# Kernel optimization log

Hardware: AMD Instinct MI355X
Metric: run time of the kernel (lower is better)

The kernel has to match this reference:

```python
import jax, jax.numpy as jnp
import numpy as np

D_BINS = 59          # cfg.cam_d
BEV_H, BEV_W = 128, 128


def setup_inputs() -> dict:
    key = jax.random.key(0)
    k = jax.random.split(key, 7)
    B, N, Cin, H, W = 4, 6, 256, 16, 44
    C = 80  # cfg.cam_bev_c
    img_feats = jax.random.normal(k[0], (B, N, Cin, H, W), dtype=jnp.float32)
    rots = jax.random.normal(k[1], (B, N, 3, 3), dtype=jnp.float32)
    trans = jax.random.normal(k[2], (B, N, 3), dtype=jnp.float32)
    intrins = jax.random.normal(k[3], (B, N, 3, 3), dtype=jnp.float32)
    # 1x1 conv == per-pixel linear layer: weight (D+C, Cin), bias (D+C,)
    w_depth = jax.random.normal(k[4], (D_BINS + C, Cin), dtype=jnp.float32) / np.sqrt(Cin)
    b_depth = jnp.zeros((D_BINS + C,), dtype=jnp.float32)
    # projected BEV grid indices (what get_geometry produces via randint)
    geom = jax.random.randint(k[5], (B, N, D_BINS, H, W, 2), 0, BEV_H, dtype=jnp.int32)
    return {"img_feats": img_feats, "rots": rots, "trans": trans,
            "intrins": intrins, "w_depth": w_depth, "b_depth": b_depth,
            "geom": geom}


def reference(img_feats, rots, trans, intrins, w_depth, b_depth, geom):
    B, N, Cin, H, W = img_feats.shape
    C = w_depth.shape[0] - D_BINS
    # depth_net: 1x1 conv -> (B, N, D+C, H, W)
    x = jnp.einsum('bnchw,oc->bnohw', img_feats, w_depth) + b_depth[None, None, :, None, None]
    depth = jax.nn.softmax(x[:, :, :D_BINS], axis=2)          # (B,N,D,H,W)
    context = x[:, :, D_BINS:]                                 # (B,N,C,H,W)
    # outer product: (B,N,D,C,H,W) -> (B,N,D,H,W,C)
    frustum = depth[:, :, :, None] * context[:, :, None]
    frustum = jnp.transpose(frustum, (0, 1, 2, 4, 5, 3))
    # voxel pooling: scatter-add frustum points into BEV grid by geom indices
    cell = geom[..., 0] * BEV_W + geom[..., 1]                 # (B,N,D,H,W)
    flat_idx = (jnp.arange(B, dtype=jnp.int32)[:, None] * (BEV_H * BEV_W)
                + cell.reshape(B, -1)).reshape(-1)
    bev = jax.ops.segment_sum(frustum.reshape(-1, C), flat_idx,
                              num_segments=B * BEV_H * BEV_W)
    return bev.reshape(B, BEV_H, BEV_W, C).transpose(0, 3, 1, 2)  # (B,C,bev_h,bev_w)
```

## Files before the change

kernel.cpp:

```cpp
#include <hip/hip_runtime.h>
#include <hip/hip_bf16.h>
#include <math.h>

#define D_BINS 59
#define CTX    80
#define O_TOT  139
#define K_CIN  256
#define PIXELS 704
#define BNPAIR 24
#define BEVHW  16384
#define NBATCH 4

#define NTILE   128
#define NBUCKET (NBATCH * NTILE)
#define TCELLS  128

#define NBLK    264
#define SEGS    66
#define EPB     (64 * D_BINS)

#define CAP     2816
#define CAPP    (CAP + TCELLS * 7)

#define CTX_OFF    0
#define CTX_F      (BNPAIR * PIXELS * CTX / 2)
#define CNTMAT_OFF (CTX_OFF + CTX_F)
#define OFSMAT_OFF (CNTMAT_OFF + NBLK * NTILE)
#define PLIST_OFF  (OFSMAT_OFF + NBLK * NTILE)

__global__ __launch_bounds__(256) void gemm_fused(
    const float* __restrict__ img,
    const float* __restrict__ w,
    const float* __restrict__ bias,
    const int*   __restrict__ geom,
    __hip_bfloat16* __restrict__ ctx,
    uint2*       __restrict__ plist,
    int*         __restrict__ cntmat,
    int*         __restrict__ ofsmat)
{
    __shared__ float As[16][64];
    __shared__ float Bs[16][64];
    __shared__ float red[16][64];
    __shared__ int lh[NTILE], lofs[NTILE], lcur[NTILE], sscan[NTILE];

    const int tid = threadIdx.x;
    const int tx  = tid & 15;
    const int ty  = tid >> 4;
    const int bn  = blockIdx.z;
    const int by  = blockIdx.y;
    const int o0  = by * 64;
    const int p0  = blockIdx.x * 64;

    const float* imgbn = img + (size_t)bn * K_CIN * PIXELS;

    float acc[4][4];
#pragma unroll
    for (int i = 0; i < 4; ++i)
#pragma unroll
        for (int j = 0; j < 4; ++j) acc[i][j] = 0.f;

    const int a_ol = tid >> 2;
    const int a_kc = (tid & 3) * 4;
    const int b_kl = tid >> 4;
    const int b_p4 = (tid & 15) * 4;

    for (int kt = 0; kt < K_CIN; kt += 16) {
        {
            const int o = o0 + a_ol;
            float4 v = make_float4(0.f, 0.f, 0.f, 0.f);
            if (o < O_TOT) v = *(const float4*)&w[(size_t)o * K_CIN + kt + a_kc];
            As[a_kc + 0][a_ol] = v.x;
            As[a_kc + 1][a_ol] = v.y;
            As[a_kc + 2][a_ol] = v.z;
            As[a_kc + 3][a_ol] = v.w;
        }
        *(float4*)&Bs[b_kl][b_p4] =
            *(const float4*)&imgbn[(size_t)(kt + b_kl) * PIXELS + p0 + b_p4];
        __syncthreads();

#pragma unroll
        for (int kk = 0; kk < 16; ++kk) {
            const float4 a = *(const float4*)&As[kk][ty * 4];
            const float4 b = *(const float4*)&Bs[kk][tx * 4];
            const float av[4] = {a.x, a.y, a.z, a.w};
            const float bv[4] = {b.x, b.y, b.z, b.w};
#pragma unroll
            for (int i = 0; i < 4; ++i)
#pragma unroll
                for (int j = 0; j < 4; ++j)
                    acc[i][j] += av[i] * bv[j];
        }
        __syncthreads();
    }

    if (by == 0) {
        float bvv[4];
#pragma unroll
        for (int i = 0; i < 4; ++i) bvv[i] = bias[ty * 4 + i];
#pragma unroll
        for (int i = 0; i < 4; ++i)
#pragma unroll
            for (int j = 0; j < 4; ++j) acc[i][j] += bvv[i];

        float pm[4] = {-INFINITY, -INFINITY, -INFINITY, -INFINITY};
#pragma unroll
        for (int i = 0; i < 4; ++i) {
            if (ty * 4 + i < D_BINS) {
#pragma unroll
                for (int j = 0; j < 4; ++j) pm[j] = fmaxf(pm[j], acc[i][j]);
            }
        }
#pragma unroll
        for (int j = 0; j < 4; ++j) red[ty][tx * 4 + j] = pm[j];
        __syncthreads();
        float gm[4] = {-INFINITY, -INFINITY, -INFINITY, -INFINITY};
        for (int t = 0; t < 15; ++t) {
            const float4 r = *(const float4*)&red[t][tx * 4];
            gm[0] = fmaxf(gm[0], r.x); gm[1] = fmaxf(gm[1], r.y);
            gm[2] = fmaxf(gm[2], r.z); gm[3] = fmaxf(gm[3], r.w);
        }
        __syncthreads();
        float ps[4] = {0.f, 0.f, 0.f, 0.f};
#pragma unroll
        for (int i = 0; i < 4; ++i) {
            if (ty * 4 + i < D_BINS) {
#pragma unroll
                for (int j = 0; j < 4; ++j) {
                    const float e = __expf(acc[i][j] - gm[j]);
                    acc[i][j] = e;
                    ps[j] += e;
                }
            }
        }
#pragma unroll
        for (int j = 0; j < 4; ++j) red[ty][tx * 4 + j] = (ty < 15) ? ps[j] : 0.f;
        if (tid < NTILE) lh[tid] = 0;
        __syncthreads();
        float gs[4] = {0.f, 0.f, 0.f, 0.f};
        for (int t = 0; t < 15; ++t) {
            const float4 r = *(const float4*)&red[t][tx * 4];
            gs[0] += r.x; gs[1] += r.y; gs[2] += r.z; gs[3] += r.w;
        }
        float inv[4];
#pragma unroll
        for (int j = 0; j < 4; ++j) inv[j] = 1.f / gs[j];

        const int2* g2 = (const int2*)geom;
        unsigned bc[4][4];
#pragma unroll
        for (int i = 0; i < 4; ++i) {
            const int o = ty * 4 + i;
            if (o < D_BINS) {
                const size_t gidx = ((size_t)(bn * D_BINS + o)) * PIXELS + p0 + tx * 4;
                const int4 ga = *(const int4*)&g2[gidx];
                const int4 gb = *(const int4*)&g2[gidx + 2];
                const int gx[4] = {ga.x, ga.z, gb.x, gb.z};
                const int gy[4] = {ga.y, ga.w, gb.y, gb.w};
#pragma unroll
                for (int j = 0; j < 4; ++j) {
                    const int tile = (gx[j] >> 3) * 8 + (gy[j] >> 4);
                    const int cell = (gx[j] & 7) * 16 + (gy[j] & 15);
                    bc[i][j] = (unsigned)((tile << 7) | cell);
                    atomicAdd(&lh[tile], 1);
                }
            }
        }
        __syncthreads();

        if (tid < NTILE) sscan[tid] = lh[tid];
        __syncthreads();
#pragma unroll
        for (int off = 1; off < NTILE; off <<= 1) {
            const int t = (tid < NTILE && tid >= off) ? sscan[tid - off] : 0;
            __syncthreads();
            if (tid < NTILE) sscan[tid] += t;
            __syncthreads();
        }
        const int blk = bn * 11 + blockIdx.x;
        if (tid < NTILE) {
            const int excl = sscan[tid] - lh[tid];
            lofs[tid] = excl;
            lcur[tid] = 0;
            cntmat[(size_t)blk * NTILE + tid] = lh[tid];
            ofsmat[(size_t)blk * NTILE + tid] = excl;
        }
        __syncthreads();

        uint2* dst = plist + (size_t)blk * EPB;
#pragma unroll
        for (int j = 0; j < 4; ++j) {
            const unsigned ctxoff = (unsigned)((bn * PIXELS + p0 + tx * 4 + j) * CTX);
#pragma unroll
            for (int i = 0; i < 4; ++i) {
                const int o = ty * 4 + i;
                if (o < D_BINS) {
                    const unsigned u = bc[i][j];
                    const int t = (int)(u >> 7);
                    const int pos = lofs[t] + atomicAdd(&lcur[t], 1);
                    dst[pos] = make_uint2(__float_as_uint(acc[i][j] * inv[j]),
                                          (ctxoff << 7) | (u & 127u));
                }
            }
        }

#pragma unroll
        for (int i = 0; i < 4; ++i) {
            const int o = ty * 4 + i;
            if (o >= D_BINS) {
                const int c = o - D_BINS;
                __hip_bfloat16* cdst = ctx + ((size_t)bn * PIXELS + p0 + tx * 4) * CTX + c;
#pragma unroll
                for (int j = 0; j < 4; ++j)
                    cdst[(size_t)j * CTX] = __float2bfloat16(acc[i][j]);
            }
        }
    } else {
#pragma unroll
        for (int i = 0; i < 4; ++i) {
            const int o = o0 + ty * 4 + i;
            if (o >= O_TOT) continue;
            const float bvv = bias[o];
            const int c = o - D_BINS;
            __hip_bfloat16* cdst = ctx + ((size_t)bn * PIXELS + p0 + tx * 4) * CTX + c;
#pragma unroll
            for (int j = 0; j < 4; ++j)
                cdst[(size_t)j * CTX] = __float2bfloat16(acc[i][j] + bvv);
        }
    }
}

__global__ __launch_bounds__(1024) void gather_kernel(
    const uint2* __restrict__ plist,
    const int*   __restrict__ cntmat,
    const int*   __restrict__ ofsmat,
    const unsigned short* __restrict__ ctx,
    float*       __restrict__ out)
{
    __shared__ float sacc[CTX][TCELLS + 1];
    __shared__ uint2 bufB[CAPP];
    __shared__ int sg[128];
    __shared__ int segcnt[SEGS], segofs[SEGS];
    __shared__ int cellcnt[TCELLS], celloff[TCELLS], cellcur[TCELLS], sc[TCELLS];
    uint2* bufA = (uint2*)sacc;

    const int tid    = threadIdx.x;
    const int wv     = tid >> 6;
    const int lane   = tid & 63;
    const int bucket = blockIdx.x;
    const int b      = bucket >> 7;
    const int tile   = bucket & 127;
    const int blk0   = b * SEGS;

    if (tid < 128) {
        const int c = (tid < SEGS) ? cntmat[(size_t)(blk0 + tid) * NTILE + tile] : 0;
        sg[tid] = c;
        if (tid < SEGS) segcnt[tid] = c;
    }
    __syncthreads();
#pragma unroll
    for (int off = 1; off < 128; off <<= 1) {
        const int t = (tid < 128 && tid >= off) ? sg[tid - off] : 0;
        __syncthreads();
        if (tid < 128) sg[tid] += t;
        __syncthreads();
    }
    if (tid < SEGS) segofs[tid] = sg[tid] - segcnt[tid];
    __syncthreads();
    const int total = sg[127];

    for (int sgi = wv; sgi < SEGS; sgi += 16) {
        const int n = segcnt[sgi];
        if (!n) continue;
        const int dstb = segofs[sgi];
        const uint2* sp = plist + (size_t)(blk0 + sgi) * EPB
                          + ofsmat[(size_t)(blk0 + sgi) * NTILE + tile];
        for (int i = lane; i < n; i += 64) {
            const int d = dstb + i;
            if (d < CAP) bufA[d] = sp[i];
        }
    }
    const int ncap = (total < CAP) ? total : CAP;
    __syncthreads();

    if (tid < TCELLS) cellcnt[tid] = 0;
    __syncthreads();
    for (int i = tid; i < ncap; i += 1024)
        atomicAdd(&cellcnt[bufA[i].y & 127u], 1);
    __syncthreads();
    if (tid < TCELLS) sc[tid] = (cellcnt[tid] + 7) & ~7;
    __syncthreads();
#pragma unroll
    for (int off = 1; off < TCELLS; off <<= 1) {
        const int t = (tid < TCELLS && tid >= off) ? sc[tid - off] : 0;
        __syncthreads();
        if (tid < TCELLS) sc[tid] += t;
        __syncthreads();
    }
    if (tid < TCELLS) {
        celloff[tid] = sc[tid] - ((cellcnt[tid] + 7) & ~7);
        cellcur[tid] = 0;
    }
    __syncthreads();
    const int padtotal = sc[TCELLS - 1];
    for (int i = tid; i < padtotal; i += 1024) bufB[i] = make_uint2(0u, 0u);
    __syncthreads();
    for (int i = tid; i < ncap; i += 1024) {
        const uint2 e = bufA[i];
        const int c = (int)(e.y & 127u);
        bufB[celloff[c] + atomicAdd(&cellcur[c], 1)] = e;
    }
    __syncthreads();

    for (int c = wv; c < TCELLS; c += 16) {
        const int s0 = celloff[c];
        const int pc = (cellcnt[c] + 7) & ~7;
        float a0 = 0.f, a1 = 0.f;
        for (int i = 0; i < pc; i += 8) {
            uint2 e[8];
#pragma unroll
            for (int r = 0; r < 8; ++r) e[r] = bufB[s0 + i + r];
            if (lane < 40) {
                unsigned u[8];
#pragma unroll
                for (int r = 0; r < 8; ++r)
                    u[r] = *(const unsigned*)(ctx + (e[r].y >> 7) + 2 * lane);
#pragma unroll
                for (int r = 0; r < 8; ++r) {
                    const float d  = __uint_as_float(e[r].x);
                    const float f0 = __uint_as_float(u[r] << 16);
                    const float f1 = __uint_as_float(u[r] & 0xffff0000u);
                    a0 += d * f0;
                    a1 += d * f1;
                }
            }
        }
        if (lane < 40) {
            sacc[2 * lane][c]     = a0;
            sacc[2 * lane + 1][c] = a1;
        }
    }

    if (total > CAP) {
        for (int sgi = 0; sgi < SEGS; ++sgi) {
            const int dstb = segofs[sgi];
            const int n    = segcnt[sgi];
            if (dstb + n <= CAP) continue;
            const uint2* sp = plist + (size_t)(blk0 + sgi) * EPB
                              + ofsmat[(size_t)(blk0 + sgi) * NTILE + tile];
            const int i0 = (CAP > dstb) ? (CAP - dstb) : 0;
            for (int i = i0; i < n; ++i) {
                const uint2 e = sp[i];
                const int c = (int)(e.y & 127u);
                if ((c & 15) == wv && lane < 40) {
                    const unsigned u = *(const unsigned*)(ctx + (e.y >> 7) + 2 * lane);
                    const float dep = __uint_as_float(e.x);
                    sacc[2 * lane][c]     += dep * __uint_as_float(u << 16);
                    sacc[2 * lane + 1][c] += dep * __uint_as_float(u & 0xffff0000u);
                }
            }
        }
    }
    __syncthreads();

    const int tl = bucket & 127;
    const int tr = tl >> 3;
    const int tc = tl & 7;
    const int c0  = tid >> 4;
    const int col = tid & 15;
#pragma unroll
    for (int cc = c0; cc < CTX; cc += 64) {
#pragma unroll
        for (int r = 0; r < 8; ++r) {
            out[((size_t)(b * CTX + cc)) * BEVHW + (tr * 8 + r) * 128 + tc * 16 + col]
                = sacc[cc][r * 16 + col];
        }
    }
}

extern "C" void kernel_launch(void* const* d_in, const int* in_sizes, int n_in,
                              void* d_out, int out_size, void* d_ws, size_t ws_size,
                              hipStream_t stream)
{
    const float* img  = (const float*)d_in[0];
    const float* w    = (const float*)d_in[4];
    const float* bias = (const float*)d_in[5];
    const int*   geom = (const int*)d_in[6];
    float*       out  = (float*)d_out;

    float* ws     = (float*)d_ws;
    __hip_bfloat16* ctx = (__hip_bfloat16*)(ws + CTX_OFF);
    int*   cntmat = (int*)(ws + CNTMAT_OFF);
    int*   ofsmat = (int*)(ws + OFSMAT_OFF);
    uint2* plist  = (uint2*)(ws + PLIST_OFF);

    {
        dim3 grid(11, 3, BNPAIR);
        gemm_fused<<<grid, 256, 0, stream>>>(img, w, bias, geom, ctx,
                                             plist, cntmat, ofsmat);
    }
    gather_kernel<<<NBUCKET, 1024, 0, stream>>>(plist, cntmat, ofsmat,
                                                (const unsigned short*)ctx, out);
}
```

Measured before the change: 146.2 us.

## Use split-bf16 MFMA for depth-net GEMM with per-block full output rows

```diff
diff --git a/kernel.cpp b/kernel.cpp
--- a/kernel.cpp
+++ b/kernel.cpp
@@ -5,6 +5,7 @@
 #define D_BINS 59
 #define CTX    80
 #define O_TOT  139
+#define O_PAD  144
 #define K_CIN  256
 #define PIXELS 704
 #define BNPAIR 24
@@ -15,22 +16,48 @@
 #define NBUCKET (NBATCH * NTILE)
 #define TCELLS  128
 
-#define NBLK    264
-#define SEGS    66
-#define EPB     (64 * D_BINS)
-
-#define CAP     2816
-#define CAPP    (CAP + TCELLS * 7)
-
-#define CTX_OFF    0
+#define PXT    32
+#define NPXT   22
+#define NBLK   (BNPAIR * NPXT)
+#define SEGS   (6 * NPXT)
+#define EPB    (PXT * D_BINS)
+
+#define CAP    2816
+#define CAPP   (CAP + TCELLS * 7)
+
+#define WHL_F      36864
+#define CTX_OFF    (WHL_F)
 #define CTX_F      (BNPAIR * PIXELS * CTX / 2)
 #define CNTMAT_OFF (CTX_OFF + CTX_F)
 #define OFSMAT_OFF (CNTMAT_OFF + NBLK * NTILE)
 #define PLIST_OFF  (OFSMAT_OFF + NBLK * NTILE)
 
-__global__ __launch_bounds__(256) void gemm_fused(
+typedef __attribute__((ext_vector_type(8))) short bf16x8;
+typedef __attribute__((ext_vector_type(4))) float f32x4;
+
+__device__ __forceinline__ unsigned short f2bf(float v) {
+    __hip_bfloat16 h = __float2bfloat16(v);
+    return *reinterpret_cast<unsigned short*>(&h);
+}
+__device__ __forceinline__ float bf2f(unsigned short u) {
+    return __uint_as_float(((unsigned)u) << 16);
+}
+
+__global__ __launch_bounds__(256) void wsplit_kernel(
+    const float* __restrict__ w, unsigned short* __restrict__ whl)
+{
+    const int row = blockIdx.x;
+    const int col = threadIdx.x;
+    const float v = (row < O_TOT) ? w[(size_t)row * K_CIN + col] : 0.f;
+    const unsigned short hi = f2bf(v);
+    const unsigned short lo = f2bf(v - bf2f(hi));
+    whl[row * K_CIN + col]            = hi;
+    whl[36864 + row * K_CIN + col]    = lo;
+}
+
+__global__ __launch_bounds__(128) void gemm_fused(
     const float* __restrict__ img,
-    const float* __restrict__ w,
+    const unsigned short* __restrict__ whl,
     const float* __restrict__ bias,
     const int*   __restrict__ geom,
     __hip_bfloat16* __restrict__ ctx,
@@ -38,194 +65,177 @@
     int*         __restrict__ cntmat,
     int*         __restrict__ ofsmat)
 {
-    __shared__ float As[16][64];
-    __shared__ float Bs[16][64];
-    __shared__ float red[16][64];
+    __shared__ __align__(16) unsigned char sW[2][O_PAD * 64];
+    __shared__ __align__(16) unsigned char sI[2][PXT * 64];
+    __shared__ float sbias[O_PAD];
     __shared__ int lh[NTILE], lofs[NTILE], lcur[NTILE], sscan[NTILE];
 
-    const int tid = threadIdx.x;
-    const int tx  = tid & 15;
-    const int ty  = tid >> 4;
-    const int bn  = blockIdx.z;
-    const int by  = blockIdx.y;
-    const int o0  = by * 64;
-    const int p0  = blockIdx.x * 64;
+    const int tid  = threadIdx.x;
+    const int lane = tid & 63;
+    const int wv   = tid >> 6;
+    const int bn   = blockIdx.y;
+    const int p0   = blockIdx.x * PXT;
+
+    sbias[tid] = bias[tid];
+    if (tid < 16) sbias[128 + tid] = (128 + tid < O_TOT) ? bias[128 + tid] : 0.f;
+    lh[tid] = 0;
 
     const float* imgbn = img + (size_t)bn * K_CIN * PIXELS;
 
-    float acc[4][4];
-#pragma unroll
-    for (int i = 0; i < 4; ++i)
-#pragma unroll
-        for (int j = 0; j < 4; ++j) acc[i][j] = 0.f;
-
-    const int a_ol = tid >> 2;
-    const int a_kc = (tid & 3) * 4;
-    const int b_kl = tid >> 4;
-    const int b_p4 = (tid & 15) * 4;
-
-    for (int kt = 0; kt < K_CIN; kt += 16) {
+    f32x4 acc[9];
+#pragma unroll
+    for (int t = 0; t < 9; ++t) acc[t] = (f32x4){0.f, 0.f, 0.f, 0.f};
+
+    const int k2  = tid >> 3;
+    const int px4 = (tid & 7) * 4;
+
+    for (int ks = 0; ks < 8; ++ks) {
+        const int k0 = ks * 32;
+        __syncthreads();
+#pragma unroll
+        for (int pl = 0; pl < 2; ++pl) {
+            for (int c = tid; c < 576; c += 128) {
+                const int row = c >> 2, g = c & 3;
+                const int gs  = g ^ ((row >> 1) & 3);
+                *(float4*)&sW[pl][row * 64 + gs * 16] =
+                    *(const float4*)&whl[pl * 36864 + row * K_CIN + k0 + g * 8];
+            }
+        }
         {
-            const int o = o0 + a_ol;
-            float4 v = make_float4(0.f, 0.f, 0.f, 0.f);
-            if (o < O_TOT) v = *(const float4*)&w[(size_t)o * K_CIN + kt + a_kc];
-            As[a_kc + 0][a_ol] = v.x;
-            As[a_kc + 1][a_ol] = v.y;
-            As[a_kc + 2][a_ol] = v.z;
-            As[a_kc + 3][a_ol] = v.w;
-        }
-        *(float4*)&Bs[b_kl][b_p4] =
-            *(const float4*)&imgbn[(size_t)(kt + b_kl) * PIXELS + p0 + b_p4];
-        __syncthreads();
-
-#pragma unroll
-        for (int kk = 0; kk < 16; ++kk) {
-            const float4 a = *(const float4*)&As[kk][ty * 4];
-            const float4 b = *(const float4*)&Bs[kk][tx * 4];
-            const float av[4] = {a.x, a.y, a.z, a.w};
-            const float bv[4] = {b.x, b.y, b.z, b.w};
-#pragma unroll
-            for (int i = 0; i < 4; ++i)
-#pragma unroll
-                for (int j = 0; j < 4; ++j)
-                    acc[i][j] += av[i] * bv[j];
-        }
-        __syncthreads();
-    }
-
-    if (by == 0) {
-        float bvv[4];
-#pragma unroll
-        for (int i = 0; i < 4; ++i) bvv[i] = bias[ty * 4 + i];
-#pragma unroll
-        for (int i = 0; i < 4; ++i)
-#pragma unroll
-            for (int j = 0; j < 4; ++j) acc[i][j] += bvv[i];
-
-        float pm[4] = {-INFINITY, -INFINITY, -INFINITY, -INFINITY};
-#pragma unroll
-        for (int i = 0; i < 4; ++i) {
-            if (ty * 4 + i < D_BINS) {
-#pragma unroll
-                for (int j = 0; j < 4; ++j) pm[j] = fmaxf(pm[j], acc[i][j]);
-            }
-        }
-#pragma unroll
-        for (int j = 0; j < 4; ++j) red[ty][tx * 4 + j] = pm[j];
-        __syncthreads();
-        float gm[4] = {-INFINITY, -INFINITY, -INFINITY, -INFINITY};
-        for (int t = 0; t < 15; ++t) {
-            const float4 r = *(const float4*)&red[t][tx * 4];
-            gm[0] = fmaxf(gm[0], r.x); gm[1] = fmaxf(gm[1], r.y);
-            gm[2] = fmaxf(gm[2], r.z); gm[3] = fmaxf(gm[3], r.w);
-        }
-        __syncthreads();
-        float ps[4] = {0.f, 0.f, 0.f, 0.f};
-#pragma unroll
-        for (int i = 0; i < 4; ++i) {
-            if (ty * 4 + i < D_BINS) {
-#pragma unroll
-                for (int j = 0; j < 4; ++j) {
-                    const float e = __expf(acc[i][j] - gm[j]);
-                    acc[i][j] = e;
-                    ps[j] += e;
-                }
-            }
-        }
-#pragma unroll
-        for (int j = 0; j < 4; ++j) red[ty][tx * 4 + j] = (ty < 15) ? ps[j] : 0.f;
-        if (tid < NTILE) lh[tid] = 0;
-        __syncthreads();
-        float gs[4] = {0.f, 0.f, 0.f, 0.f};
-        for (int t = 0; t < 15; ++t) {
-            const float4 r = *(const float4*)&red[t][tx * 4];
-            gs[0] += r.x; gs[1] += r.y; gs[2] += r.z; gs[3] += r.w;
-        }
-        float inv[4];
-#pragma unroll
-        for (int j = 0; j < 4; ++j) inv[j] = 1.f / gs[j];
-
-        const int2* g2 = (const int2*)geom;
-        unsigned bc[4][4];
-#pragma unroll
-        for (int i = 0; i < 4; ++i) {
-            const int o = ty * 4 + i;
+            const float4 v0 = *(const float4*)&imgbn[(size_t)(k0 + 2 * k2) * PIXELS + p0 + px4];
+            const float4 v1 = *(const float4*)&imgbn[(size_t)(k0 + 2 * k2 + 1) * PIXELS + p0 + px4];
+            const float a0[4] = {v0.x, v0.y, v0.z, v0.w};
+            const float a1[4] = {v1.x, v1.y, v1.z, v1.w};
+#pragma unroll
+            for (int j = 0; j < 4; ++j) {
+                const int px  = px4 + j;
+                const int gs  = (k2 >> 2) ^ ((px >> 1) & 3);
+                const int off = px * 64 + gs * 16 + 4 * (k2 & 3);
+                const unsigned short h0 = f2bf(a0[j]);
+                const unsigned short h1 = f2bf(a1[j]);
+                const unsigned short l0 = f2bf(a0[j] - bf2f(h0));
+                const unsigned short l1 = f2bf(a1[j] - bf2f(h1));
+                *(unsigned*)&sI[0][off] = (unsigned)h0 | ((unsigned)h1 << 16);
+                *(unsigned*)&sI[1][off] = (unsigned)l0 | ((unsigned)l1 << 16);
+            }
+        }
+        __syncthreads();
+        const int m = lane & 15;
+        const int g = lane >> 4;
+        const int bpx = wv * 16 + m;
+        const int bgs = g ^ ((bpx >> 1) & 3);
+        const bf16x8 bhi = *(const bf16x8*)&sI[0][bpx * 64 + bgs * 16];
+        const bf16x8 blo = *(const bf16x8*)&sI[1][bpx * 64 + bgs * 16];
+#pragma unroll
+        for (int t = 0; t < 9; ++t) {
+            const int row = t * 16 + m;
+            const int ags = g ^ ((row >> 1) & 3);
+            const bf16x8 ahi = *(const bf16x8*)&sW[0][row * 64 + ags * 16];
+            const bf16x8 alo = *(const bf16x8*)&sW[1][row * 64 + ags * 16];
+            acc[t] = __builtin_amdgcn_mfma_f32_16x16x32_bf16(ahi, bhi, acc[t], 0, 0, 0);
+            acc[t] = __builtin_amdgcn_mfma_f32_16x16x32_bf16(ahi, blo, acc[t], 0, 0, 0);
+            acc[t] = __builtin_amdgcn_mfma_f32_16x16x32_bf16(alo, bhi, acc[t], 0, 0, 0);
+        }
+    }
+
+    const int m   = lane & 15;
+    const int q   = lane >> 4;
+    const int px_local = wv * 16 + m;
+    const int pxg = p0 + px_local;
+
+#pragma unroll
+    for (int t = 0; t < 9; ++t)
+#pragma unroll
+        for (int r = 0; r < 4; ++r) acc[t][r] += sbias[t * 16 + q * 4 + r];
+
+    float gm = -INFINITY;
+#pragma unroll
+    for (int t = 0; t < 4; ++t)
+#pragma unroll
+        for (int r = 0; r < 4; ++r)
+            if (16 * t + 4 * q + r < D_BINS) gm = fmaxf(gm, acc[t][r]);
+    gm = fmaxf(gm, __shfl_xor(gm, 16));
+    gm = fmaxf(gm, __shfl_xor(gm, 32));
+    float ls = 0.f;
+#pragma unroll
+    for (int t = 0; t < 4; ++t)
+#pragma unroll
+        for (int r = 0; r < 4; ++r)
+            if (16 * t + 4 * q + r < D_BINS) {
+                const float e = __expf(acc[t][r] - gm);
+                acc[t][r] = e;
+                ls += e;
+            }
+    ls += __shfl_xor(ls, 16);
+    ls += __shfl_xor(ls, 32);
+    const float inv = 1.f / ls;
+
+    __syncthreads();
+
+    unsigned short* sctx = (unsigned short*)&sW[0][0];
+    const int2* g2 = (const int2*)geom;
+    unsigned bc[4][4];
+#pragma unroll
+    for (int t = 0; t < 4; ++t)
+#pragma unroll
+        for (int r = 0; r < 4; ++r) {
+            const int o = 16 * t + 4 * q + r;
             if (o < D_BINS) {
-                const size_t gidx = ((size_t)(bn * D_BINS + o)) * PIXELS + p0 + tx * 4;
-                const int4 ga = *(const int4*)&g2[gidx];
-                const int4 gb = *(const int4*)&g2[gidx + 2];
-                const int gx[4] = {ga.x, ga.z, gb.x, gb.z};
-                const int gy[4] = {ga.y, ga.w, gb.y, gb.w};
-#pragma unroll
-                for (int j = 0; j < 4; ++j) {
-                    const int tile = (gx[j] >> 3) * 8 + (gy[j] >> 4);
-                    const int cell = (gx[j] & 7) * 16 + (gy[j] & 15);
-                    bc[i][j] = (unsigned)((tile << 7) | cell);
-                    atomicAdd(&lh[tile], 1);
-                }
-            }
-        }
-        __syncthreads();
-
-        if (tid < NTILE) sscan[tid] = lh[tid];
-        __syncthreads();
-#pragma unroll
-        for (int off = 1; off < NTILE; off <<= 1) {
-            const int t = (tid < NTILE && tid >= off) ? sscan[tid - off] : 0;
-            __syncthreads();
-            if (tid < NTILE) sscan[tid] += t;
-            __syncthreads();
-        }
-        const int blk = bn * 11 + blockIdx.x;
-        if (tid < NTILE) {
-            const int excl = sscan[tid] - lh[tid];
-            lofs[tid] = excl;
-            lcur[tid] = 0;
-            cntmat[(size_t)blk * NTILE + tid] = lh[tid];
-            ofsmat[(size_t)blk * NTILE + tid] = excl;
-        }
-        __syncthreads();
-
-        uint2* dst = plist + (size_t)blk * EPB;
-#pragma unroll
-        for (int j = 0; j < 4; ++j) {
-            const unsigned ctxoff = (unsigned)((bn * PIXELS + p0 + tx * 4 + j) * CTX);
-#pragma unroll
-            for (int i = 0; i < 4; ++i) {
-                const int o = ty * 4 + i;
-                if (o < D_BINS) {
-                    const unsigned u = bc[i][j];
-                    const int t = (int)(u >> 7);
-                    const int pos = lofs[t] + atomicAdd(&lcur[t], 1);
-                    dst[pos] = make_uint2(__float_as_uint(acc[i][j] * inv[j]),
-                                          (ctxoff << 7) | (u & 127u));
-                }
-            }
-        }
-
-#pragma unroll
-        for (int i = 0; i < 4; ++i) {
-            const int o = ty * 4 + i;
-            if (o >= D_BINS) {
-                const int c = o - D_BINS;
-                __hip_bfloat16* cdst = ctx + ((size_t)bn * PIXELS + p0 + tx * 4) * CTX + c;
-#pragma unroll
-                for (int j = 0; j < 4; ++j)
-                    cdst[(size_t)j * CTX] = __float2bfloat16(acc[i][j]);
-            }
-        }
-    } else {
-#pragma unroll
-        for (int i = 0; i < 4; ++i) {
-            const int o = o0 + ty * 4 + i;
-            if (o >= O_TOT) continue;
-            const float bvv = bias[o];
-            const int c = o - D_BINS;
-            __hip_bfloat16* cdst = ctx + ((size_t)bn * PIXELS + p0 + tx * 4) * CTX + c;
-#pragma unroll
-            for (int j = 0; j < 4; ++j)
-                cdst[(size_t)j * CTX] = __float2bfloat16(acc[i][j] + bvv);
-        }
+                const int2 gg = g2[((size_t)(bn * D_BINS + o)) * PIXELS + pxg];
+                const int tile = (gg.x >> 3) * 8 + (gg.y >> 4);
+                const int cell = (gg.x & 7) * 16 + (gg.y & 15);
+                bc[t][r] = (unsigned)((tile << 7) | cell);
+                atomicAdd(&lh[tile], 1);
+            }
+        }
+#pragma unroll
+    for (int t = 3; t < 9; ++t)
+#pragma unroll
+        for (int r = 0; r < 4; ++r) {
+            const int c = 16 * t + 4 * q + r - D_BINS;
+            if (c >= 0 && c < CTX) sctx[px_local * CTX + c] = f2bf(acc[t][r]);
+        }
+    __syncthreads();
+
+    sscan[tid] = lh[tid];
+    __syncthreads();
+#pragma unroll
+    for (int off = 1; off < NTILE; off <<= 1) {
+        const int t = (tid >= off) ? sscan[tid - off] : 0;
+        __syncthreads();
+        sscan[tid] += t;
+        __syncthreads();
+    }
+    const int blk = bn * NPXT + blockIdx.x;
+    {
+        const int excl = sscan[tid] - lh[tid];
+        lofs[tid] = excl;
+        lcur[tid] = 0;
+        cntmat[(size_t)blk * NTILE + tid] = lh[tid];
+        ofsmat[(size_t)blk * NTILE + tid] = excl;
+    }
+    __syncthreads();
+
+    uint2* dst = plist + (size_t)blk * EPB;
+    const unsigned ctxoff = (unsigned)((bn * PIXELS + pxg) * CTX);
+#pragma unroll
+    for (int t = 0; t < 4; ++t)
+#pragma unroll
+        for (int r = 0; r < 4; ++r) {
+            const int o = 16 * t + 4 * q + r;
+            if (o < D_BINS) {
+                const unsigned u = bc[t][r];
+                const int tl = (int)(u >> 7);
+                const int pos = lofs[tl] + atomicAdd(&lcur[tl], 1);
+                dst[pos] = make_uint2(__float_as_uint(acc[t][r] * inv),
+                                      (ctxoff << 7) | (u & 127u));
+            }
+        }
+    {
+        const char* sb = (const char*)sctx;
+        char* gb = (char*)ctx + ((size_t)(bn * PIXELS) + p0) * CTX * 2;
+        for (int i = tid; i < PXT * CTX * 2 / 16; i += 128)
+            *(float4*)(gb + i * 16) = *(const float4*)(sb + i * 16);
     }
 }
 
@@ -238,7 +248,7 @@
 {
     __shared__ float sacc[CTX][TCELLS + 1];
     __shared__ uint2 bufB[CAPP];
-    __shared__ int sg[128];
+    __shared__ int sg[256];
     __shared__ int segcnt[SEGS], segofs[SEGS];
     __shared__ int cellcnt[TCELLS], celloff[TCELLS], cellcur[TCELLS], sc[TCELLS];
     uint2* bufA = (uint2*)sacc;
@@ -251,32 +261,36 @@
     const int tile   = bucket & 127;
     const int blk0   = b * SEGS;
 
-    if (tid < 128) {
+    if (tid < 256) {
         const int c = (tid < SEGS) ? cntmat[(size_t)(blk0 + tid) * NTILE + tile] : 0;
         sg[tid] = c;
         if (tid < SEGS) segcnt[tid] = c;
     }
     __syncthreads();
 #pragma unroll
-    for (int off = 1; off < 128; off <<= 1) {
-        const int t = (tid < 128 && tid >= off) ? sg[tid - off] : 0;
-        __syncthreads();
-        if (tid < 128) sg[tid] += t;
+    for (int off = 1; off < 256; off <<= 1) {
+        const int t = (tid < 256 && tid >= off) ? sg[tid - off] : 0;
+        __syncthreads();
+        if (tid < 256) sg[tid] += t;
         __syncthreads();
     }
     if (tid < SEGS) segofs[tid] = sg[tid] - segcnt[tid];
     __syncthreads();
-    const int total = sg[127];
-
-    for (int sgi = wv; sgi < SEGS; sgi += 16) {
-        const int n = segcnt[sgi];
-        if (!n) continue;
-        const int dstb = segofs[sgi];
-        const uint2* sp = plist + (size_t)(blk0 + sgi) * EPB
-                          + ofsmat[(size_t)(blk0 + sgi) * NTILE + tile];
-        for (int i = lane; i < n; i += 64) {
-            const int d = dstb + i;
-            if (d < CAP) bufA[d] = sp[i];
+    const int total = sg[255];
+
+    {
+        const int sub = lane >> 4;
+        const int sl  = lane & 15;
+        for (int sgi = wv * 4 + sub; sgi < SEGS; sgi += 64) {
+            const int n = segcnt[sgi];
+            if (!n) continue;
+            const int dstb = segofs[sgi];
+            const uint2* sp = plist + (size_t)(blk0 + sgi) * EPB
+                              + ofsmat[(size_t)(blk0 + sgi) * NTILE + tile];
+            for (int i = sl; i < n; i += 16) {
+                const int d = dstb + i;
+                if (d < CAP) bufA[d] = sp[i];
+            }
         }
     }
     const int ncap = (total < CAP) ? total : CAP;
@@ -327,10 +341,8 @@
 #pragma unroll
                 for (int r = 0; r < 8; ++r) {
                     const float d  = __uint_as_float(e[r].x);
-                    const float f0 = __uint_as_float(u[r] << 16);
-                    const float f1 = __uint_as_float(u[r] & 0xffff0000u);
-                    a0 += d * f0;
-                    a1 += d * f1;
+                    a0 += d * __uint_as_float(u[r] << 16);
+                    a1 += d * __uint_as_float(u[r] & 0xffff0000u);
                 }
             }
         }
@@ -387,17 +399,21 @@
     const int*   geom = (const int*)d_in[6];
     float*       out  = (float*)d_out;
 
-    float* ws     = (float*)d_ws;
+    float* ws = (float*)d_ws;
+    unsigned short* whl = (unsigned short*)ws;
     __hip_bfloat16* ctx = (__hip_bfloat16*)(ws + CTX_OFF);
     int*   cntmat = (int*)(ws + CNTMAT_OFF);
     int*   ofsmat = (int*)(ws + OFSMAT_OFF);
     uint2* plist  = (uint2*)(ws + PLIST_OFF);
 
+    wsplit_kernel<<<O_PAD, 256, 0, stream>>>(w, whl);
+
     {
-        dim3 grid(11, 3, BNPAIR);
-        gemm_fused<<<grid, 256, 0, stream>>>(img, w, bias, geom, ctx,
+        dim3 grid(NPXT, BNPAIR);
+        gemm_fused<<<grid, 128, 0, stream>>>(img, whl, bias, geom, ctx,
                                              plist, cntmat, ofsmat);
     }
+
     gather_kernel<<<NBUCKET, 1024, 0, stream>>>(plist, cntmat, ofsmat,
                                                 (const unsigned short*)ctx, out);
 }
```

New measurement: 144.5 us. About the same (-1.2%).
